# Performance work log

Hardware: AMD Instinct MI355X
Metric: run time of the kernel (lower is better)

Reference implementation:

```python
import jax, jax.numpy as jnp
import numpy as np

LN10 = float(np.log(10.0))
EPS = 1e-10


def _band_e(L1, L2, R1, R2, rho1, rho2, g2p, g2m, gp, gm,
            cos1, sin1, cos2, sin2, epsexp, deltexp, epsdelexp):
    """EC-stage expected energy over the (tau, gamma) grid.
    L*,R*: (S,N) real; rho*: (S,N) complex -> (S, ntaus, ngammas)."""
    # first part: gamma-only terms (S,G) broadcast over taus
    first = (jnp.sum(L1 * L2, 1)[:, None] * g2p
             + jnp.sum(R1 * R2, 1)[:, None] * g2m) * epsexp
    first = first[:, None, :] + (jnp.sum(L1 * R2, 1)
                                 + jnp.sum(R1 * L2, 1))[:, None, None]
    r1r, r1i = jnp.real(rho1), jnp.imag(rho1)
    r2r, r2i = jnp.real(rho2), jnp.imag(rho2)
    # Re(rho * exp(-i*w*tau)) = Re(rho)*cos(w*tau) + Im(rho)*sin(w*tau);
    # contracting over the N frames first avoids the (S,N,ntaus) intermediate.
    sec = ((jnp.sum(L1 * r1r, 1) + jnp.sum(L2 * r2r, 1))[:, None] * cos1
           + (jnp.sum(L1 * r1i, 1) + jnp.sum(L2 * r2i, 1))[:, None] * sin1)  # (S,T)
    second = 2.0 * sec[:, :, None] * gp * epsdelexp[None]
    thr = ((jnp.sum(R1 * r1r, 1) + jnp.sum(R2 * r2r, 1))[:, None] * cos1
           + (jnp.sum(R1 * r1i, 1) + jnp.sum(R2 * r2i, 1))[:, None] * sin1)
    third = 2.0 * thr[:, :, None] * gm * epsdelexp[None]
    t1 = jnp.sum(r1r * r2r + r1i * r2i, 1)          # Re(sum rho1*conj(rho2)), (S,)
    q = jnp.sum(rho1 * rho2, 1)                     # (S,) complex
    t2 = jnp.real(q)[:, None] * cos2 + jnp.imag(q)[:, None] * sin2  # Re(q*e^{-2iwt})
    fourth = 2.0 * (t1[:, None] + deltexp[None, :] * t2)[:, :, None]
    return first - second - third + fourth


def _ec(xl_re, xl_im, xr_re, xr_im, yl_re, yl_im, yr_re, yr_im,
        cf, taus, gammas, sigma_epsilon, sigma_delta, fids, N):
    xl = xl_re + 1j * xl_im
    xr = xr_re + 1j * xr_im
    yl = yl_re + 1j * yl_im
    yr = yr_re + 1j * yr_im
    F = xl.shape[1]
    S = F - N + 1                                   # number of N-frame segments
    widx = jnp.arange(S)[:, None] + jnp.arange(N)[None, :]
    fids_np = np.asarray(fids)
    J = fids_np.shape[0]
    epsexp = jnp.exp(2.0 * LN10 ** 2 * sigma_epsilon ** 2)        # (G,)
    g2p, g2m = 10.0 ** (2.0 * gammas), 10.0 ** (-2.0 * gammas)    # (G,)
    gp, gm = 10.0 ** gammas, 10.0 ** (-gammas)
    d = []
    for i in range(J):                              # J=15 structurally distinct bands
        lo, hi = int(fids_np[i, 0]) - 1, int(fids_np[i, 1])
        c = cf[i]
        wt = c * taus
        cos1, sin1 = jnp.cos(wt), jnp.sin(wt)       # tauexp = cos - i*sin
        cos2, sin2 = jnp.cos(2.0 * wt), jnp.sin(2.0 * wt)
        deltexp = jnp.exp(-(c ** 2) * sigma_delta ** 2)           # (T,)
        epsdelexp = jnp.exp(0.5 * (LN10 ** 2 * sigma_epsilon[None, :] ** 2
                                   - (c ** 2) * sigma_delta[:, None] ** 2))  # (T,G)

        def seg(a):
            return a[lo:hi][:, widx]                # (kk,S,N) sliding windows

        def norm(s):
            L = jnp.sum(jnp.real(jnp.conj(s) * s), 0)             # (S,N)
            return L - L.mean(1, keepdims=True)

        def rho(sr, sl):
            r = jnp.sum(jnp.conj(sr) * sl, 0)                     # (S,N) complex
            return r - r.mean(1, keepdims=True)

        sxl, sxr, syl, syr = seg(xl), seg(xr), seg(yl), seg(yr)
        Lx, Rx, Ly, Ry = norm(sxl), norm(sxr), norm(syl), norm(syr)
        rhox, rhoy = rho(sxr, sxl), rho(syr, syl)
        args = (g2p, g2m, gp, gm, cos1, sin1, cos2, sin2, epsexp, deltexp, epsdelexp)
        exy = _band_e(Lx, Ly, Rx, Ry, rhoy, rhox, *args)
        exx = _band_e(Lx, Lx, Rx, Rx, rhox, rhox, *args)
        eyy = _band_e(Ly, Ly, Ry, Ry, rhoy, rhoy, *args)
        p = exy / jnp.sqrt(jnp.maximum(exx * eyy, EPS))
        d.append(jnp.max(p.reshape(S, -1), axis=1))               # max over (tau,gamma)
    return jnp.stack(d, 0)                                        # (J,S)


def setup_inputs() -> dict:
    key = jax.random.key(0)
    K, F, N, J, T, G = 128, 4000, 30, 15, 100, 40
    ks = jax.random.split(key, 8)
    names = ["xl_re", "xl_im", "xr_re", "xr_im", "yl_re", "yl_im", "yr_re", "yr_im"]
    inp = {n: 0.1 * jax.random.normal(k, (K, F), dtype=jnp.float32)
           for n, k in zip(names, ks)}
    edges = np.array([0, 3, 5, 8, 11, 15, 20, 26, 33, 41, 50, 61, 74, 89, 107, 128])
    fids = np.stack([edges[:-1] + 1, edges[1:]], axis=1).astype(np.int64)  # 1-based
    cf = 2.0 * np.pi * np.geomspace(150.0, 4000.0, J)   # centre freqs in rad/s
    taus = np.linspace(-1e-3, 1e-3, T)
    gammas = np.linspace(-1.0, 1.0, G)                  # dB/20 units
    sigma_delta = 65e-6 * (1.0 + np.abs(taus) / 1e-3)
    sigma_epsilon = np.sqrt(2.0) * (1.5 / 20.0) * (1.0 + np.abs(gammas))
    inp.update(
        cf=jnp.asarray(cf, jnp.float32),
        taus=jnp.asarray(taus, jnp.float32),
        gammas=jnp.asarray(gammas, jnp.float32),
        sigma_epsilon=jnp.asarray(sigma_epsilon, jnp.float32),
        sigma_delta=jnp.asarray(sigma_delta, jnp.float32),
        fids=jnp.asarray(fids),
        N=N,
    )
    return inp


def reference(xl_re, xl_im, xr_re, xr_im, yl_re, yl_im, yr_re, yr_im,
              cf, taus, gammas, sigma_epsilon, sigma_delta, fids, N):
    return _ec(xl_re, xl_im, xr_re, xr_im, yl_re, yl_im, yr_re, yr_im,
               cf, taus, gammas, sigma_epsilon, sigma_delta, fids, N)
```

## Files before the change

kernel.cpp:

```cpp
#include <hip/hip_runtime.h>
#include <math.h>

#define LN10_SQ 5.3018981104783984f
#define LOG2_10 3.3219280948873623f

constexpr int NWIN = 30;
constexpr int SEGS_PER_BLOCK = 64;
constexpr int NFRM = SEGS_PER_BLOCK + NWIN - 1;
constexpr int NTHREADS = 512;
constexpr int TSPLIT = 8;
constexpr int TABSTRIDE = 1024;
constexpr int TAB_RESERVE = 16384;

__global__ __launch_bounds__(256) void ec_prep(
    const float* __restrict__ xlr, const float* __restrict__ xli,
    const float* __restrict__ xrre, const float* __restrict__ xrim,
    const float* __restrict__ ylr, const float* __restrict__ yli,
    const float* __restrict__ yrre, const float* __restrict__ yrim,
    const float* __restrict__ cf, const float* __restrict__ taus,
    const float* __restrict__ gammas, const float* __restrict__ sigeps,
    const float* __restrict__ sigdel, const int* __restrict__ fids,
    float* __restrict__ ser, float* __restrict__ tab,
    int F, int T, int G, int K)
{
    const int band = blockIdx.y;
    const int tid = threadIdx.x;
    const float cw = cf[band];

    if (blockIdx.x == 0) {
        if (tid < T) {
            float tau = taus[tid];
            float wt = cw * tau;
            float sn1, cs1, sn2, cs2;
            sincosf(wt, &sn1, &cs1);
            sincosf(2.0f * wt, &sn2, &cs2);
            float sd = sigdel[tid];
            float Dt = expf(-0.5f * cw * cw * sd * sd);
            float* pa = tab + band * TABSTRIDE + tid * 4;
            pa[0] = cs1; pa[1] = sn1; pa[2] = cs2; pa[3] = sn2;
            float* pb = tab + band * TABSTRIDE + 512 + tid * 2;
            pb[0] = 2.0f * Dt; pb[1] = 2.0f * Dt * Dt;
        }
        int gg = tid - 128;
        if (gg >= 0 && gg < G) {
            float gam = gammas[gg];
            float se = sigeps[gg];
            float ee = expf(2.0f * LN10_SQ * se * se);
            float Eg = expf(0.5f * LN10_SQ * se * se);
            float* pg = tab + band * TABSTRIDE + 768 + gg * 4;
            pg[0] = exp2f(2.0f * gam * LOG2_10) * ee;
            pg[1] = exp2f(-2.0f * gam * LOG2_10) * ee;
            pg[2] = exp2f(gam * LOG2_10) * Eg;
            pg[3] = exp2f(-gam * LOG2_10) * Eg;
        }
    }

    int lo, hi;
    if (fids[1] == 0) { lo = fids[4 * band] - 1; hi = fids[4 * band + 2]; }
    else              { lo = fids[2 * band] - 1; hi = fids[2 * band + 1]; }
    lo = lo < 0 ? 0 : lo;
    hi = hi > K ? K : hi;

    const int f = blockIdx.x * 256 + tid;
    if (f >= F) return;
    float Lx = 0.f, Rx = 0.f, Ly = 0.f, Ry = 0.f;
    float rxr = 0.f, rxi = 0.f, ryr = 0.f, ryi = 0.f;
    for (int k = lo; k < hi; ++k) {
        int idx = k * F + f;
        float a = xlr[idx], b = xli[idx], c = xrre[idx], d = xrim[idx];
        Lx = fmaf(a, a, fmaf(b, b, Lx));
        Rx = fmaf(c, c, fmaf(d, d, Rx));
        rxr = fmaf(c, a, fmaf(d, b, rxr));
        rxi = fmaf(c, b, rxi) - d * a;
        float e = ylr[idx], g = yli[idx], h = yrre[idx], i2 = yrim[idx];
        Ly = fmaf(e, e, fmaf(g, g, Ly));
        Ry = fmaf(h, h, fmaf(i2, i2, Ry));
        ryr = fmaf(h, e, fmaf(i2, g, ryr));
        ryi = fmaf(h, g, ryi) - i2 * e;
    }
    float* bs = ser + (size_t)band * 8 * F;
    bs[0 * F + f] = Lx;  bs[1 * F + f] = Rx;
    bs[2 * F + f] = Ly;  bs[3 * F + f] = Ry;
    bs[4 * F + f] = rxr; bs[5 * F + f] = rxi;
    bs[6 * F + f] = ryr; bs[7 * F + f] = ryi;
}

__global__ __launch_bounds__(256) void ec_scal(
    const float* __restrict__ ser, float* __restrict__ scal, int F, int S)
{
    const int band = blockIdx.y;
    const int seg = blockIdx.x * 256 + threadIdx.x;
    if (seg >= S) return;
    const float* bs = ser + (size_t)band * 8 * F;
    float s0=0,s1=0,s2=0,s3=0,s4=0,s5=0,s6=0,s7=0;
    float c00=0,c01=0,c02=0,c03=0,c04=0,c05=0,c06=0,c07=0;
    float c11=0,c12=0,c13=0,c14=0,c15=0,c16=0,c17=0;
    float c22=0,c23=0,c24=0,c25=0,c26=0,c27=0;
    float c33=0,c34=0,c35=0,c36=0,c37=0;
    float c44=0,c45=0,c46=0,c47=0;
    float c55=0,c56=0,c57=0;
    float c66=0,c67=0;
    float c77=0;
    #pragma unroll 5
    for (int n = 0; n < NWIN; ++n) {
        float v0 = bs[0*F+seg+n], v1 = bs[1*F+seg+n];
        float v2 = bs[2*F+seg+n], v3 = bs[3*F+seg+n];
        float v4 = bs[4*F+seg+n], v5 = bs[5*F+seg+n];
        float v6 = bs[6*F+seg+n], v7 = bs[7*F+seg+n];
        s0+=v0; s1+=v1; s2+=v2; s3+=v3; s4+=v4; s5+=v5; s6+=v6; s7+=v7;
        c00=fmaf(v0,v0,c00); c01=fmaf(v0,v1,c01); c02=fmaf(v0,v2,c02); c03=fmaf(v0,v3,c03);
        c04=fmaf(v0,v4,c04); c05=fmaf(v0,v5,c05); c06=fmaf(v0,v6,c06); c07=fmaf(v0,v7,c07);
        c11=fmaf(v1,v1,c11); c12=fmaf(v1,v2,c12); c13=fmaf(v1,v3,c13); c14=fmaf(v1,v4,c14);
        c15=fmaf(v1,v5,c15); c16=fmaf(v1,v6,c16); c17=fmaf(v1,v7,c17);
        c22=fmaf(v2,v2,c22); c23=fmaf(v2,v3,c23); c24=fmaf(v2,v4,c24); c25=fmaf(v2,v5,c25);
        c26=fmaf(v2,v6,c26); c27=fmaf(v2,v7,c27);
        c33=fmaf(v3,v3,c33); c34=fmaf(v3,v4,c34); c35=fmaf(v3,v5,c35); c36=fmaf(v3,v6,c36);
        c37=fmaf(v3,v7,c37);
        c44=fmaf(v4,v4,c44); c45=fmaf(v4,v5,c45); c46=fmaf(v4,v6,c46); c47=fmaf(v4,v7,c47);
        c55=fmaf(v5,v5,c55); c56=fmaf(v5,v6,c56); c57=fmaf(v5,v7,c57);
        c66=fmaf(v6,v6,c66); c67=fmaf(v6,v7,c67);
        c77=fmaf(v7,v7,c77);
    }
    const float rN = 1.0f / (float)NWIN;
    #define CEN(a,b) fmaf(-(s##a * rN), s##b, c##a##b)
    float t46 = CEN(4,6), t57 = CEN(5,7), t56 = CEN(5,6), t47 = CEN(4,7);
    float t44 = CEN(4,4), t55 = CEN(5,5);
    float t66 = CEN(6,6), t77 = CEN(7,7);
    float o[27];
    o[0]  = CEN(0,2);
    o[1]  = CEN(1,3);
    o[2]  = CEN(0,3) + CEN(1,2) + 2.0f*(t46+t57);
    o[3]  = CEN(0,6) + CEN(2,4);
    o[4]  = CEN(0,7) + CEN(2,5);
    o[5]  = CEN(1,6) + CEN(3,4);
    o[6]  = CEN(1,7) + CEN(3,5);
    o[7]  = t46 - t57;
    o[8]  = t56 + t47;
    o[9]  = CEN(0,0);
    o[10] = CEN(1,1);
    o[11] = 2.0f*CEN(0,1) + 2.0f*(t44+t55);
    o[12] = 2.0f*CEN(0,4);
    o[13] = 2.0f*CEN(0,5);
    o[14] = 2.0f*CEN(1,4);
    o[15] = 2.0f*CEN(1,5);
    o[16] = t44 - t55;
    o[17] = 2.0f*CEN(4,5);
    o[18] = CEN(2,2);
    o[19] = CEN(3,3);
    o[20] = 2.0f*CEN(2,3) + 2.0f*(t66+t77);
    o[21] = 2.0f*CEN(2,6);
    o[22] = 2.0f*CEN(2,7);
    o[23] = 2.0f*CEN(3,6);
    o[24] = 2.0f*CEN(3,7);
    o[25] = t66 - t77;
    o[26] = 2.0f*CEN(6,7);
    #undef CEN
    #pragma unroll
    for (int c = 0; c < 27; ++c)
        scal[((size_t)band * 27 + c) * S + seg] = o[c];
}

__global__ __launch_bounds__(NTHREADS, 1) void ec_sweep(
    const float* __restrict__ tab, const float* __restrict__ scal,
    float* __restrict__ out, int S, int T, int G)
{
    __shared__ float red[NTHREADS];

    const int tid = threadIdx.x;
    const int band = blockIdx.y;
    const int seg_base = blockIdx.x * SEGS_PER_BLOCK;

    const float4* __restrict__ tA = (const float4*)(tab + band * TABSTRIDE);
    const float2* __restrict__ tB = (const float2*)(tab + band * TABSTRIDE + 512);
    const float4* __restrict__ gT = (const float4*)(tab + band * TABSTRIDE + 768);

    const int seg = seg_base + (tid & 63);
    const int segc = seg < S ? seg : S - 1;
    const float* sp = scal + (size_t)band * 27 * S + segc;
    float A_xy  = sp[0*S],  B_xy  = sp[1*S],  base_xy = sp[2*S];
    float sc_xy = sp[3*S],  ss_xy = sp[4*S];
    float tc_xy = sp[5*S],  ts_xy = sp[6*S];
    float qr_xy = sp[7*S],  qi_xy = sp[8*S];
    float A_xx  = sp[9*S],  B_xx  = sp[10*S], base_xx = sp[11*S];
    float sc_xx = sp[12*S], ss_xx = sp[13*S];
    float tc_xx = sp[14*S], ts_xx = sp[15*S];
    float qr_xx = sp[16*S], qi_xx = sp[17*S];
    float A_yy  = sp[18*S], B_yy  = sp[19*S], base_yy = sp[20*S];
    float sc_yy = sp[21*S], ss_yy = sp[22*S];
    float tc_yy = sp[23*S], ts_yy = sp[24*S];
    float qr_yy = sp[25*S], qi_yy = sp[26*S];

    asm volatile("" : "+v"(A_xy), "+v"(B_xy), "+v"(base_xy), "+v"(sc_xy),
                      "+v"(ss_xy), "+v"(tc_xy), "+v"(ts_xy), "+v"(qr_xy),
                      "+v"(qi_xy), "+v"(A_xx), "+v"(B_xx), "+v"(base_xx),
                      "+v"(sc_xx), "+v"(ss_xx), "+v"(tc_xx), "+v"(ts_xx));
    asm volatile("" : "+v"(qr_xx), "+v"(qi_xx), "+v"(A_yy), "+v"(B_yy),
                      "+v"(base_yy), "+v"(sc_yy), "+v"(ss_yy), "+v"(tc_yy),
                      "+v"(ts_yy), "+v"(qr_yy), "+v"(qi_yy));

    const int split = tid >> 6;
    const int t0 = __builtin_amdgcn_readfirstlane((split * T) / TSPLIT);
    const int t1 = __builtin_amdgcn_readfirstlane(((split + 1) * T) / TSPLIT);

    float m = -3.4e38f;
    for (int t = t0; t < t1; ++t) {
        float4 ta = tA[t];
        float2 tv = tB[t];
        float w1 = fmaf(tv.y, fmaf(qi_xy, ta.w, qr_xy * ta.z), base_xy);
        float u1 = fmaf(ss_xy, ta.y, sc_xy * ta.x) * tv.x;
        float v1 = fmaf(ts_xy, ta.y, tc_xy * ta.x) * tv.x;
        float w2 = fmaf(tv.y, fmaf(qi_xx, ta.w, qr_xx * ta.z), base_xx);
        float u2 = fmaf(ss_xx, ta.y, sc_xx * ta.x) * tv.x;
        float v2 = fmaf(ts_xx, ta.y, tc_xx * ta.x) * tv.x;
        float w3 = fmaf(tv.y, fmaf(qi_yy, ta.w, qr_yy * ta.z), base_yy);
        float u3 = fmaf(ss_yy, ta.y, sc_yy * ta.x) * tv.x;
        float v3 = fmaf(ts_yy, ta.y, tc_yy * ta.x) * tv.x;
        #pragma unroll 4
        for (int g = 0; g < G; ++g) {
            float4 gt = gT[g];
            float exy = fmaf(A_xy, gt.x, w1);
            exy = fmaf(B_xy, gt.y, exy);
            exy = fmaf(-u1, gt.z, exy);
            exy = fmaf(-v1, gt.w, exy);
            float exx = fmaf(A_xx, gt.x, w2);
            exx = fmaf(B_xx, gt.y, exx);
            exx = fmaf(-u2, gt.z, exx);
            exx = fmaf(-v2, gt.w, exx);
            float eyy = fmaf(A_yy, gt.x, w3);
            eyy = fmaf(B_yy, gt.y, eyy);
            eyy = fmaf(-u3, gt.z, eyy);
            eyy = fmaf(-v3, gt.w, eyy);
            float den = fmaxf(exx * eyy, 1e-10f);
            m = fmaxf(m, exy * __builtin_amdgcn_rsqf(den));
        }
    }

    red[tid] = m;
    __syncthreads();
    if (tid < SEGS_PER_BLOCK) {
        float r = red[tid];
        #pragma unroll
        for (int kk = 1; kk < TSPLIT; ++kk)
            r = fmaxf(r, red[tid + 64 * kk]);
        int sg = seg_base + tid;
        if (sg < S) out[(size_t)band * S + sg] = r;
    }
}

__global__ __launch_bounds__(NTHREADS) void ec_fused_kernel(
    const float* __restrict__ xlr, const float* __restrict__ xli,
    const float* __restrict__ xrre, const float* __restrict__ xrim,
    const float* __restrict__ ylr, const float* __restrict__ yli,
    const float* __restrict__ yrre, const float* __restrict__ yrim,
    const float* __restrict__ cf, const float* __restrict__ taus,
    const float* __restrict__ gammas, const float* __restrict__ sigeps,
    const float* __restrict__ sigdel, const int* __restrict__ fids,
    float* __restrict__ out, int F, int S, int T, int G, int K)
{
    __shared__ float4 ttabA[128];
    __shared__ float2 ttabB[128];
    __shared__ float4 gtab[64];
    __shared__ float  sser[8][96];
    __shared__ float  scal[27][64];
    __shared__ float  red[NTHREADS];

    const int tid = threadIdx.x;
    const int band = blockIdx.y;
    const int seg_base = blockIdx.x * SEGS_PER_BLOCK;
    const float cw = cf[band];

    int lo, hi;
    if (fids[1] == 0) { lo = fids[4 * band] - 1; hi = fids[4 * band + 2]; }
    else              { lo = fids[2 * band] - 1; hi = fids[2 * band + 1]; }
    lo = lo < 0 ? 0 : lo;
    hi = hi > K ? K : hi;

    {
        int tt = tid - 128;
        if (tt >= 0 && tt < T) {
            float tau = taus[tt];
            float wt = cw * tau;
            float sn1, cs1, sn2, cs2;
            sincosf(wt, &sn1, &cs1);
            sincosf(2.0f * wt, &sn2, &cs2);
            float sd = sigdel[tt];
            float Dt = expf(-0.5f * cw * cw * sd * sd);
            ttabA[tt] = make_float4(cs1, sn1, cs2, sn2);
            ttabB[tt] = make_float2(2.0f * Dt, 2.0f * Dt * Dt);
        }
        int gg = tid - 256;
        if (gg >= 0 && gg < G) {
            float gam = gammas[gg];
            float se = sigeps[gg];
            float ee = expf(2.0f * LN10_SQ * se * se);
            float Eg = expf(0.5f * LN10_SQ * se * se);
            gtab[gg] = make_float4(exp2f(2.0f*gam*LOG2_10)*ee, exp2f(-2.0f*gam*LOG2_10)*ee,
                                   exp2f(gam*LOG2_10)*Eg, exp2f(-gam*LOG2_10)*Eg);
        }
    }

    if (tid < NFRM) {
        int j = tid;
        int f = seg_base + j;
        float Lx = 0.f, Rx = 0.f, Ly = 0.f, Ry = 0.f;
        float rxr = 0.f, rxi = 0.f, ryr = 0.f, ryi = 0.f;
        if (f < F) {
            for (int k = lo; k < hi; ++k) {
                int idx = k * F + f;
                float a = xlr[idx], b = xli[idx], c = xrre[idx], d = xrim[idx];
                Lx = fmaf(a, a, fmaf(b, b, Lx));
                Rx = fmaf(c, c, fmaf(d, d, Rx));
                rxr = fmaf(c, a, fmaf(d, b, rxr));
                rxi = fmaf(c, b, rxi) - d * a;
                float e = ylr[idx], g = yli[idx], h = yrre[idx], i2 = yrim[idx];
                Ly = fmaf(e, e, fmaf(g, g, Ly));
                Ry = fmaf(h, h, fmaf(i2, i2, Ry));
                ryr = fmaf(h, e, fmaf(i2, g, ryr));
                ryi = fmaf(h, g, ryi) - i2 * e;
            }
        }
        sser[0][j] = Lx;  sser[1][j] = Rx;
        sser[2][j] = Ly;  sser[3][j] = Ry;
        sser[4][j] = rxr; sser[5][j] = rxi;
        sser[6][j] = ryr; sser[7][j] = ryi;
    }
    __syncthreads();

    if (tid < SEGS_PER_BLOCK) {
        const int segL = tid;
        float s0=0,s1=0,s2=0,s3=0,s4=0,s5=0,s6=0,s7=0;
        float c00=0,c01=0,c02=0,c03=0,c04=0,c05=0,c06=0,c07=0;
        float c11=0,c12=0,c13=0,c14=0,c15=0,c16=0,c17=0;
        float c22=0,c23=0,c24=0,c25=0,c26=0,c27=0;
        float c33=0,c34=0,c35=0,c36=0,c37=0;
        float c44=0,c45=0,c46=0,c47=0;
        float c55=0,c56=0,c57=0;
        float c66=0,c67=0;
        float c77=0;
        #pragma unroll 5
        for (int n = 0; n < NWIN; ++n) {
            float v0 = sser[0][segL + n], v1 = sser[1][segL + n];
            float v2 = sser[2][segL + n], v3 = sser[3][segL + n];
            float v4 = sser[4][segL + n], v5 = sser[5][segL + n];
            float v6 = sser[6][segL + n], v7 = sser[7][segL + n];
            s0+=v0; s1+=v1; s2+=v2; s3+=v3; s4+=v4; s5+=v5; s6+=v6; s7+=v7;
            c00=fmaf(v0,v0,c00); c01=fmaf(v0,v1,c01); c02=fmaf(v0,v2,c02); c03=fmaf(v0,v3,c03);
            c04=fmaf(v0,v4,c04); c05=fmaf(v0,v5,c05); c06=fmaf(v0,v6,c06); c07=fmaf(v0,v7,c07);
            c11=fmaf(v1,v1,c11); c12=fmaf(v1,v2,c12); c13=fmaf(v1,v3,c13); c14=fmaf(v1,v4,c14);
            c15=fmaf(v1,v5,c15); c16=fmaf(v1,v6,c16); c17=fmaf(v1,v7,c17);
            c22=fmaf(v2,v2,c22); c23=fmaf(v2,v3,c23); c24=fmaf(v2,v4,c24); c25=fmaf(v2,v5,c25);
            c26=fmaf(v2,v6,c26); c27=fmaf(v2,v7,c27);
            c33=fmaf(v3,v3,c33); c34=fmaf(v3,v4,c34); c35=fmaf(v3,v5,c35); c36=fmaf(v3,v6,c36);
            c37=fmaf(v3,v7,c37);
            c44=fmaf(v4,v4,c44); c45=fmaf(v4,v5,c45); c46=fmaf(v4,v6,c46); c47=fmaf(v4,v7,c47);
            c55=fmaf(v5,v5,c55); c56=fmaf(v5,v6,c56); c57=fmaf(v5,v7,c57);
            c66=fmaf(v6,v6,c66); c67=fmaf(v6,v7,c67);
            c77=fmaf(v7,v7,c77);
        }
        const float rN = 1.0f / (float)NWIN;
        #define CEN(a,b) fmaf(-(s##a * rN), s##b, c##a##b)
        float t46 = CEN(4,6), t57 = CEN(5,7), t56 = CEN(5,6), t47 = CEN(4,7);
        scal[0][segL] = CEN(0,2);
        scal[1][segL] = CEN(1,3);
        scal[2][segL] = CEN(0,3) + CEN(1,2) + 2.0f*(t46+t57);
        scal[3][segL] = CEN(0,6) + CEN(2,4);
        scal[4][segL] = CEN(0,7) + CEN(2,5);
        scal[5][segL] = CEN(1,6) + CEN(3,4);
        scal[6][segL] = CEN(1,7) + CEN(3,5);
        scal[7][segL] = t46 - t57;
        scal[8][segL] = t56 + t47;
        float t44 = CEN(4,4), t55 = CEN(5,5);
        scal[9][segL]  = CEN(0,0);
        scal[10][segL] = CEN(1,1);
        scal[11][segL] = 2.0f*CEN(0,1) + 2.0f*(t44+t55);
        scal[12][segL] = 2.0f*CEN(0,4);
        scal[13][segL] = 2.0f*CEN(0,5);
        scal[14][segL] = 2.0f*CEN(1,4);
        scal[15][segL] = 2.0f*CEN(1,5);
        scal[16][segL] = t44 - t55;
        scal[17][segL] = 2.0f*CEN(4,5);
        float t66 = CEN(6,6), t77 = CEN(7,7);
        scal[18][segL] = CEN(2,2);
        scal[19][segL] = CEN(3,3);
        scal[20][segL] = 2.0f*CEN(2,3) + 2.0f*(t66+t77);
        scal[21][segL] = 2.0f*CEN(2,6);
        scal[22][segL] = 2.0f*CEN(2,7);
        scal[23][segL] = 2.0f*CEN(3,6);
        scal[24][segL] = 2.0f*CEN(3,7);
        scal[25][segL] = t66 - t77;
        scal[26][segL] = 2.0f*CEN(6,7);
        #undef CEN
    }
    __syncthreads();

    const int seg = tid & (SEGS_PER_BLOCK - 1);
    const int split = tid >> 6;
    float A_xy = scal[0][seg],  B_xy = scal[1][seg],  base_xy = scal[2][seg];
    float sc_xy = scal[3][seg], ss_xy = scal[4][seg];
    float tc_xy = scal[5][seg], ts_xy = scal[6][seg];
    float qr_xy = scal[7][seg], qi_xy = scal[8][seg];
    float A_xx = scal[9][seg],  B_xx = scal[10][seg], base_xx = scal[11][seg];
    float sc_xx = scal[12][seg], ss_xx = scal[13][seg];
    float tc_xx = scal[14][seg], ts_xx = scal[15][seg];
    float qr_xx = scal[16][seg], qi_xx = scal[17][seg];
    float A_yy = scal[18][seg], B_yy = scal[19][seg], base_yy = scal[20][seg];
    float sc_yy = scal[21][seg], ss_yy = scal[22][seg];
    float tc_yy = scal[23][seg], ts_yy = scal[24][seg];
    float qr_yy = scal[25][seg], qi_yy = scal[26][seg];

    const int t0 = __builtin_amdgcn_readfirstlane((split * T) / TSPLIT);
    const int t1 = __builtin_amdgcn_readfirstlane(((split + 1) * T) / TSPLIT);

    float m = -3.4e38f;
    for (int t = t0; t < t1; ++t) {
        float4 ta = ttabA[t];
        float2 tv = ttabB[t];
        float w1 = fmaf(tv.y, fmaf(qi_xy, ta.w, qr_xy * ta.z), base_xy);
        float u1 = fmaf(ss_xy, ta.y, sc_xy * ta.x) * tv.x;
        float v1 = fmaf(ts_xy, ta.y, tc_xy * ta.x) * tv.x;
        float w2 = fmaf(tv.y, fmaf(qi_xx, ta.w, qr_xx * ta.z), base_xx);
        float u2 = fmaf(ss_xx, ta.y, sc_xx * ta.x) * tv.x;
        float v2 = fmaf(ts_xx, ta.y, tc_xx * ta.x) * tv.x;
        float w3 = fmaf(tv.y, fmaf(qi_yy, ta.w, qr_yy * ta.z), base_yy);
        float u3 = fmaf(ss_yy, ta.y, sc_yy * ta.x) * tv.x;
        float v3 = fmaf(ts_yy, ta.y, tc_yy * ta.x) * tv.x;
        #pragma unroll 4
        for (int g = 0; g < G; ++g) {
            float4 gt = gtab[g];
            float exy = fmaf(A_xy, gt.x, w1);
            exy = fmaf(B_xy, gt.y, exy);
            exy = fmaf(-u1, gt.z, exy);
            exy = fmaf(-v1, gt.w, exy);
            float exx = fmaf(A_xx, gt.x, w2);
            exx = fmaf(B_xx, gt.y, exx);
            exx = fmaf(-u2, gt.z, exx);
            exx = fmaf(-v2, gt.w, exx);
            float eyy = fmaf(A_yy, gt.x, w3);
            eyy = fmaf(B_yy, gt.y, eyy);
            eyy = fmaf(-u3, gt.z, eyy);
            eyy = fmaf(-v3, gt.w, eyy);
            float den = fmaxf(exx * eyy, 1e-10f);
            m = fmaxf(m, exy * __builtin_amdgcn_rsqf(den));
        }
    }

    red[tid] = m;
    __syncthreads();
    if (tid < SEGS_PER_BLOCK) {
        float r = red[tid];
        #pragma unroll
        for (int kk = 1; kk < TSPLIT; ++kk)
            r = fmaxf(r, red[tid + 64 * kk]);
        int sg = seg_base + tid;
        if (sg < S) out[(size_t)band * S + sg] = r;
    }
}

extern "C" void kernel_launch(void* const* d_in, const int* in_sizes, int n_in,
                              void* d_out, int out_size, void* d_ws, size_t ws_size,
                              hipStream_t stream) {
    const float* xlr  = (const float*)d_in[0];
    const float* xli  = (const float*)d_in[1];
    const float* xrre = (const float*)d_in[2];
    const float* xrim = (const float*)d_in[3];
    const float* ylr  = (const float*)d_in[4];
    const float* yli  = (const float*)d_in[5];
    const float* yrre = (const float*)d_in[6];
    const float* yrim = (const float*)d_in[7];
    const float* cfp  = (const float*)d_in[8];
    const float* taus = (const float*)d_in[9];
    const float* gammas = (const float*)d_in[10];
    const float* sigeps = (const float*)d_in[11];
    const float* sigdel = (const float*)d_in[12];
    const int*   fids = (const int*)d_in[13];

    const int J = in_sizes[8];
    const int T = in_sizes[9];
    const int G = in_sizes[10];
    const int S = out_size / J;
    const int F = S + NWIN - 1;
    const int K = in_sizes[0] / F;

    const size_t ser_f  = (size_t)J * 8 * F;
    const size_t scal_f = (size_t)J * 27 * S;
    const size_t need   = (TAB_RESERVE + ser_f + scal_f) * sizeof(float);

    if (ws_size >= need && T <= 128 && G <= 64) {
        float* tab  = (float*)d_ws;
        float* ser  = tab + TAB_RESERVE;
        float* scal = ser + ser_f;
        dim3 b1(256), g1((F + 255) / 256, J);
        ec_prep<<<g1, b1, 0, stream>>>(xlr, xli, xrre, xrim, ylr, yli, yrre, yrim,
                                       cfp, taus, gammas, sigeps, sigdel, fids,
                                       ser, tab, F, T, G, K);
        dim3 b2(256), g2((S + 255) / 256, J);
        ec_scal<<<g2, b2, 0, stream>>>(ser, scal, F, S);
        dim3 b3(NTHREADS), g3((S + SEGS_PER_BLOCK - 1) / SEGS_PER_BLOCK, J);
        ec_sweep<<<g3, b3, 0, stream>>>(tab, scal, (float*)d_out, S, T, G);
    } else {
        dim3 b(NTHREADS), g((S + SEGS_PER_BLOCK - 1) / SEGS_PER_BLOCK, J);
        ec_fused_kernel<<<g, b, 0, stream>>>(xlr, xli, xrre, xrim, ylr, yli, yrre, yrim,
                                             cfp, taus, gammas, sigeps, sigdel,
                                             fids, (float*)d_out, F, S, T, G, K);
    }
}
```

Before: 120.4 us.

## Interchange tau and gamma loops in sweep with register-blocked tau chunks

Rewrites the ec_sweep inner loops. Each thread now precomputes the tau-dependent terms for a chunk of up to 7 taus, then a second chunk of 6, and keeps them in registers. It then iterates over gammas once per chunk, so each gamma table load and the gamma-only A*g.x+B*g.y partial sums are shared across all taus in the chunk. This cuts per-point FMAs and repeated loads of the gamma table. The cost is higher register pressure, and the code hard-codes coverage of 13 taus per split with clamped duplicate indices. Tau ranges longer than 13 per split, which T up to 128 still allows, would be silently skipped.

After: 114.3 us. -5.1%, faster.

```diff
diff --git a/kernel.cpp b/kernel.cpp
--- a/kernel.cpp
+++ b/kernel.cpp
@@ -160,6 +160,47 @@
         scal[((size_t)band * 27 + c) * S + seg] = o[c];
 }
 
+#define SWEEP_CHUNK(NCH, TBASE)                                               \
+  {                                                                           \
+    float cw1[NCH], cu1[NCH], cv1[NCH];                                       \
+    float cw2[NCH], cu2[NCH], cv2[NCH];                                       \
+    float cw3[NCH], cu3[NCH], cv3[NCH];                                       \
+    _Pragma("unroll")                                                         \
+    for (int i = 0; i < (NCH); ++i) {                                         \
+      int t = (TBASE) + i; t = t < t1 ? t : t1 - 1;     \
+      float4 ta = tA[t]; float2 tv = tB[t];                                   \
+      cw1[i] = fmaf(tv.y, fmaf(qi_xy, ta.w, qr_xy * ta.z), base_xy);          \
+      cu1[i] = fmaf(ss_xy, ta.y, sc_xy * ta.x) * tv.x;                        \
+      cv1[i] = fmaf(ts_xy, ta.y, tc_xy * ta.x) * tv.x;                        \
+      cw2[i] = fmaf(tv.y, fmaf(qi_xx, ta.w, qr_xx * ta.z), base_xx);          \
+      cu2[i] = fmaf(ss_xx, ta.y, sc_xx * ta.x) * tv.x;                        \
+      cv2[i] = fmaf(ts_xx, ta.y, tc_xx * ta.x) * tv.x;                        \
+      cw3[i] = fmaf(tv.y, fmaf(qi_yy, ta.w, qr_yy * ta.z), base_yy);          \
+      cu3[i] = fmaf(ss_yy, ta.y, sc_yy * ta.x) * tv.x;                        \
+      cv3[i] = fmaf(ts_yy, ta.y, tc_yy * ta.x) * tv.x;                        \
+    }                                                                         \
+    _Pragma("unroll")                                                         \
+    for (int i = 0; i < (NCH); ++i) {                                         \
+      asm volatile("" : "+v"(cw1[i]), "+v"(cu1[i]), "+v"(cv1[i]),             \
+                        "+v"(cw2[i]), "+v"(cu2[i]), "+v"(cv2[i]),             \
+                        "+v"(cw3[i]), "+v"(cu3[i]), "+v"(cv3[i]));            \
+    }                                                                         \
+    for (int g = 0; g < G; ++g) {                                             \
+      float4 gt = gT[g];                               \
+      float E1 = fmaf(B_xy, gt.y, A_xy * gt.x);                               \
+      float E2 = fmaf(B_xx, gt.y, A_xx * gt.x);                               \
+      float E3 = fmaf(B_yy, gt.y, A_yy * gt.x);                               \
+      _Pragma("unroll")                                                       \
+      for (int i = 0; i < (NCH); ++i) {                                       \
+        float exy = fmaf(-cv1[i], gt.w, fmaf(-cu1[i], gt.z, E1 + cw1[i]));    \
+        float exx = fmaf(-cv2[i], gt.w, fmaf(-cu2[i], gt.z, E2 + cw2[i]));    \
+        float eyy = fmaf(-cv3[i], gt.w, fmaf(-cu3[i], gt.z, E3 + cw3[i]));    \
+        float den = fmaxf(exx * eyy, 1e-10f);                                 \
+        m = fmaxf(m, exy * __builtin_amdgcn_rsqf(den));                       \
+      }                                                                       \
+    }                                                                         \
+  }
+
 __global__ __launch_bounds__(NTHREADS, 1) void ec_sweep(
     const float* __restrict__ tab, const float* __restrict__ scal,
     float* __restrict__ out, int S, int T, int G)
@@ -203,37 +244,8 @@
     const int t1 = __builtin_amdgcn_readfirstlane(((split + 1) * T) / TSPLIT);
 
     float m = -3.4e38f;
-    for (int t = t0; t < t1; ++t) {
-        float4 ta = tA[t];
-        float2 tv = tB[t];
-        float w1 = fmaf(tv.y, fmaf(qi_xy, ta.w, qr_xy * ta.z), base_xy);
-        float u1 = fmaf(ss_xy, ta.y, sc_xy * ta.x) * tv.x;
-        float v1 = fmaf(ts_xy, ta.y, tc_xy * ta.x) * tv.x;
-        float w2 = fmaf(tv.y, fmaf(qi_xx, ta.w, qr_xx * ta.z), base_xx);
-        float u2 = fmaf(ss_xx, ta.y, sc_xx * ta.x) * tv.x;
-        float v2 = fmaf(ts_xx, ta.y, tc_xx * ta.x) * tv.x;
-        float w3 = fmaf(tv.y, fmaf(qi_yy, ta.w, qr_yy * ta.z), base_yy);
-        float u3 = fmaf(ss_yy, ta.y, sc_yy * ta.x) * tv.x;
-        float v3 = fmaf(ts_yy, ta.y, tc_yy * ta.x) * tv.x;
-        #pragma unroll 4
-        for (int g = 0; g < G; ++g) {
-            float4 gt = gT[g];
-            float exy = fmaf(A_xy, gt.x, w1);
-            exy = fmaf(B_xy, gt.y, exy);
-            exy = fmaf(-u1, gt.z, exy);
-            exy = fmaf(-v1, gt.w, exy);
-            float exx = fmaf(A_xx, gt.x, w2);
-            exx = fmaf(B_xx, gt.y, exx);
-            exx = fmaf(-u2, gt.z, exx);
-            exx = fmaf(-v2, gt.w, exx);
-            float eyy = fmaf(A_yy, gt.x, w3);
-            eyy = fmaf(B_yy, gt.y, eyy);
-            eyy = fmaf(-u3, gt.z, eyy);
-            eyy = fmaf(-v3, gt.w, eyy);
-            float den = fmaxf(exx * eyy, 1e-10f);
-            m = fmaxf(m, exy * __builtin_amdgcn_rsqf(den));
-        }
-    }
+    SWEEP_CHUNK(7, t0)
+    if (t0 + 7 < t1) SWEEP_CHUNK(6, t0 + 7)
 
     red[tid] = m;
     __syncthreads();
@@ -485,7 +497,7 @@
     const size_t scal_f = (size_t)J * 27 * S;
     const size_t need   = (TAB_RESERVE + ser_f + scal_f) * sizeof(float);
 
-    if (ws_size >= need && T <= 128 && G <= 64) {
+    if (ws_size >= need && T <= 128 && G <= 64 && T / TSPLIT >= 8) {
         float* tab  = (float*)d_ws;
         float* ser  = tab + TAB_RESERVE;
         float* scal = ser + ser_f;
```

## Register-block 13 taus per thread and swap the sweep loops to iterate gammas outermost

Applied to the files above, without the earlier changes.

The sweep kernel now precomputes per-tau coefficients for a fixed chunk of 13 taus into registers. It then loops over gammas outermost, so each gamma table entry and the gamma-only partial sums E1/E2/E3 are shared across all taus in the chunk. This cuts redundant FMAs and LDS loads per (tau, gamma) point and gives the scheduler more independent work. Out-of-range taus are clamped to T-1, which is harmless under a max reduction. In exchange, register pressure rises sharply (over 100 live coefficient registers under 512-thread launch bounds), with a risk of spills or lower occupancy. The fast path is also limited to T between 8 and 104; other sizes fall back to the fused kernel.

Result: no change. 122.7 us (+1.9%).

```diff
diff --git a/kernel.cpp b/kernel.cpp
--- a/kernel.cpp
+++ b/kernel.cpp
@@ -200,39 +200,54 @@
 
     const int split = tid >> 6;
     const int t0 = __builtin_amdgcn_readfirstlane((split * T) / TSPLIT);
-    const int t1 = __builtin_amdgcn_readfirstlane(((split + 1) * T) / TSPLIT);
+
+    constexpr int CH = 13;
+    float cw1[CH], cu1[CH], cv1[CH];
+    float cw2[CH], cu2[CH], cv2[CH];
+    float cw3[CH], cu3[CH], cv3[CH];
+    #pragma unroll
+    for (int i = 0; i < CH; ++i) {
+        int t = t0 + i; t = t < T ? t : T - 1;
+        float4 ta = tA[t]; float2 tv = tB[t];
+        cw1[i] = fmaf(tv.y, fmaf(qi_xy, ta.w, qr_xy * ta.z), base_xy);
+        cu1[i] = fmaf(ss_xy, ta.y, sc_xy * ta.x) * tv.x;
+        cv1[i] = fmaf(ts_xy, ta.y, tc_xy * ta.x) * tv.x;
+        cw2[i] = fmaf(tv.y, fmaf(qi_xx, ta.w, qr_xx * ta.z), base_xx);
+        cu2[i] = fmaf(ss_xx, ta.y, sc_xx * ta.x) * tv.x;
+        cv2[i] = fmaf(ts_xx, ta.y, tc_xx * ta.x) * tv.x;
+        cw3[i] = fmaf(tv.y, fmaf(qi_yy, ta.w, qr_yy * ta.z), base_yy);
+        cu3[i] = fmaf(ss_yy, ta.y, sc_yy * ta.x) * tv.x;
+        cv3[i] = fmaf(ts_yy, ta.y, tc_yy * ta.x) * tv.x;
+    }
+    #pragma unroll
+    for (int i = 0; i < CH; ++i) {
+        asm volatile("" : "+v"(cw1[i]), "+v"(cu1[i]), "+v"(cv1[i]),
+                          "+v"(cw2[i]), "+v"(cu2[i]), "+v"(cv2[i]),
+                          "+v"(cw3[i]), "+v"(cu3[i]), "+v"(cv3[i]));
+    }
 
     float m = -3.4e38f;
-    for (int t = t0; t < t1; ++t) {
-        float4 ta = tA[t];
-        float2 tv = tB[t];
-        float w1 = fmaf(tv.y, fmaf(qi_xy, ta.w, qr_xy * ta.z), base_xy);
-        float u1 = fmaf(ss_xy, ta.y, sc_xy * ta.x) * tv.x;
-        float v1 = fmaf(ts_xy, ta.y, tc_xy * ta.x) * tv.x;
-        float w2 = fmaf(tv.y, fmaf(qi_xx, ta.w, qr_xx * ta.z), base_xx);
-        float u2 = fmaf(ss_xx, ta.y, sc_xx * ta.x) * tv.x;
-        float v2 = fmaf(ts_xx, ta.y, tc_xx * ta.x) * tv.x;
-        float w3 = fmaf(tv.y, fmaf(qi_yy, ta.w, qr_yy * ta.z), base_yy);
-        float u3 = fmaf(ss_yy, ta.y, sc_yy * ta.x) * tv.x;
-        float v3 = fmaf(ts_yy, ta.y, tc_yy * ta.x) * tv.x;
-        #pragma unroll 4
-        for (int g = 0; g < G; ++g) {
-            float4 gt = gT[g];
-            float exy = fmaf(A_xy, gt.x, w1);
-            exy = fmaf(B_xy, gt.y, exy);
-            exy = fmaf(-u1, gt.z, exy);
-            exy = fmaf(-v1, gt.w, exy);
-            float exx = fmaf(A_xx, gt.x, w2);
-            exx = fmaf(B_xx, gt.y, exx);
-            exx = fmaf(-u2, gt.z, exx);
-            exx = fmaf(-v2, gt.w, exx);
-            float eyy = fmaf(A_yy, gt.x, w3);
-            eyy = fmaf(B_yy, gt.y, eyy);
-            eyy = fmaf(-u3, gt.z, eyy);
-            eyy = fmaf(-v3, gt.w, eyy);
+    for (int g = 0; g < G; ++g) {
+        float4 gt = gT[g];
+        float E1 = fmaf(B_xy, gt.y, A_xy * gt.x);
+        float E2 = fmaf(B_xx, gt.y, A_xx * gt.x);
+        float E3 = fmaf(B_yy, gt.y, A_yy * gt.x);
+        float p[CH];
+        #pragma unroll
+        for (int i = 0; i < CH; ++i) {
+            float exy = fmaf(-cv1[i], gt.w, fmaf(-cu1[i], gt.z, E1 + cw1[i]));
+            float exx = fmaf(-cv2[i], gt.w, fmaf(-cu2[i], gt.z, E2 + cw2[i]));
+            float eyy = fmaf(-cv3[i], gt.w, fmaf(-cu3[i], gt.z, E3 + cw3[i]));
             float den = fmaxf(exx * eyy, 1e-10f);
-            m = fmaxf(m, exy * __builtin_amdgcn_rsqf(den));
-        }
+            p[i] = exy * __builtin_amdgcn_rsqf(den);
+        }
+        float q0 = fmaxf(fmaxf(p[0], p[1]), p[2]);
+        float q1 = fmaxf(fmaxf(p[3], p[4]), p[5]);
+        float q2 = fmaxf(fmaxf(p[6], p[7]), p[8]);
+        float q3 = fmaxf(fmaxf(p[9], p[10]), p[11]);
+        float q4 = fmaxf(fmaxf(q0, q1), p[12]);
+        float q5 = fmaxf(fmaxf(q2, q3), m);
+        m = fmaxf(q4, q5);
     }
 
     red[tid] = m;
@@ -485,7 +500,7 @@
     const size_t scal_f = (size_t)J * 27 * S;
     const size_t need   = (TAB_RESERVE + ser_f + scal_f) * sizeof(float);
 
-    if (ws_size >= need && T <= 128 && G <= 64) {
+    if (ws_size >= need && T >= TSPLIT && T <= 104 && G <= 64) {
         float* tab  = (float*)d_ws;
         float* ser  = tab + TAB_RESERVE;
         float* scal = ser + ser_f;
```
